# Performance work log

Measured on AMD Instinct MI355X. Metric: run time of the kernel, lower is better.

## Reference

```python
import jax, jax.numpy as jnp
import numpy as np

N_NODES = 50000
N_EDGES = 1600000
IN_DIM = 64 + 2 + 64   # protein + spatial + lri
HID = 64
OUT_DIM = 32
NUM_GRAPHS = 64
NEG_SLOPE = 0.2  # PyG GATConv default negative_slope


def _gat(x, src, dst, W, a_src, a_dst, bias):
    """PyG-style GATConv: x' = xW per head, per-edge attention with
    LeakyReLU + scatter-softmax over incoming edges, weighted scatter-sum.
    Heads are concatenated (concat=True default)."""
    N = x.shape[0]
    H, C = a_src.shape
    xp = (x @ W).reshape(N, H, C)                      # [N,H,C]
    al_src = jnp.sum(xp * a_src, axis=-1)              # [N,H]
    al_dst = jnp.sum(xp * a_dst, axis=-1)              # [N,H]
    e = jax.nn.leaky_relu(al_src[src] + al_dst[dst], NEG_SLOPE)  # [E,H]
    # numerically stable segment softmax over edges grouped by dst
    m = jax.ops.segment_max(e, dst, num_segments=N)
    ex = jnp.exp(e - m[dst])
    denom = jax.ops.segment_sum(ex, dst, num_segments=N)
    alpha = ex / denom[dst]                            # [E,H]
    out = jax.ops.segment_sum(alpha[:, :, None] * xp[src], dst, num_segments=N)
    return out.reshape(N, H * C) + bias


def setup_inputs() -> dict:
    key = jax.random.key(0)
    ks = jax.random.split(key, 16)
    def glorot(k, shape):
        fan_in = shape[0] if len(shape) == 2 else shape[-1]
        return jax.random.normal(k, shape, dtype=jnp.float32) / np.sqrt(fan_in)
    inp = {
        "protein_expr": jax.random.normal(ks[0], (N_NODES, 64), dtype=jnp.float32),
        "spatial_pos": jax.random.uniform(ks[1], (N_NODES, 2), dtype=jnp.float32),
        "lri_feats": jax.random.normal(ks[2], (N_NODES, 64), dtype=jnp.float32),
        "edge_index": jax.random.randint(ks[3], (2, N_EDGES), 0, N_NODES, dtype=jnp.int64),
        "batch": jnp.sort(jax.random.randint(ks[4], (N_NODES,), 0, NUM_GRAPHS, dtype=jnp.int64)),
        # encoder1: GATConv(IN_DIM -> HID, heads=2)
        "W1": glorot(ks[5], (IN_DIM, 2 * HID)),
        "a_src1": glorot(ks[6], (2, HID)),
        "a_dst1": glorot(ks[7], (2, HID)),
        "b1": jnp.zeros((2 * HID,), dtype=jnp.float32),
        # encoder2: GATConv(2*HID -> HID, heads=1)
        "W2": glorot(ks[8], (2 * HID, HID)),
        "a_src2": glorot(ks[9], (1, HID)),
        "a_dst2": glorot(ks[10], (1, HID)),
        "b2": jnp.zeros((HID,), dtype=jnp.float32),
        # decoder MLP
        "Wd1": glorot(ks[11], (HID, HID)),
        "bd1": jnp.zeros((HID,), dtype=jnp.float32),
        "Wd2": glorot(ks[12], (HID, OUT_DIM)),
        "bd2": jnp.zeros((OUT_DIM,), dtype=jnp.float32),
    }
    return inp


def reference(protein_expr, spatial_pos, lri_feats, edge_index, batch,
              W1, a_src1, a_dst1, b1, W2, a_src2, a_dst2, b2,
              Wd1, bd1, Wd2, bd2):
    N = protein_expr.shape[0]
    x = jnp.concatenate([protein_expr, spatial_pos, lri_feats], axis=1)  # [N, IN_DIM]
    # PyG GATConv adds self-loops by default
    loop = jnp.arange(N, dtype=edge_index.dtype)
    src = jnp.concatenate([edge_index[0], loop])
    dst = jnp.concatenate([edge_index[1], loop])
    h = _gat(x, src, dst, W1, a_src1, a_dst1, b1)   # [N, 2*HID]
    h = _gat(h, src, dst, W2, a_src2, a_dst2, b2)   # [N, HID]
    # global_mean_pool
    counts = jax.ops.segment_sum(jnp.ones((N,), h.dtype), batch, num_segments=NUM_GRAPHS)
    pooled = jax.ops.segment_sum(h, batch, num_segments=NUM_GRAPHS) / jnp.clip(counts, 1.0)[:, None]
    # decoder MLP
    d = jax.nn.relu(pooled @ Wd1 + bd1)
    return d @ Wd2 + bd2
```

## Files before the change

kernel.cpp:

```cpp
#include <hip/hip_runtime.h>
#include <hip/hip_bf16.h>

#define N_NODESC 50000
#define N_EDGESC 1600000
#define NUM_GRAPHSC 64
#define P_EPB 2048
#define SUBW 196
#define NSB 256
#define SBCAP 8192
#define POOL_REP 32
#define AGG_NB 6250

typedef __hip_bfloat16 bf16;
typedef short short8 __attribute__((ext_vector_type(8)));
typedef float floatx4 __attribute__((ext_vector_type(4)));

__device__ __forceinline__ float ldf(const void* p, long i, int fp32) {
    return fp32 ? ((const float*)p)[i] : __bfloat162float(((const bf16*)p)[i]);
}
__device__ __forceinline__ short f2s(float v) {
    bf16 h = __float2bfloat16(v);
    return *(short*)&h;
}
__device__ __forceinline__ unsigned pack2(float lo, float hi) {
    bf16 a = __float2bfloat16(lo), b = __float2bfloat16(hi);
    unsigned ua = *(unsigned short*)&a, ub = *(unsigned short*)&b;
    return (ub << 16) | ua;
}
__device__ __forceinline__ float ulo(unsigned u) { return __uint_as_float(u << 16); }
__device__ __forceinline__ float uhi(unsigned u) { return __uint_as_float(u & 0xffff0000u); }

__global__ void detect_k(const void* __restrict__ prot,
                         const void* __restrict__ eidx,
                         int* __restrict__ flags) {
    if (blockIdx.x == 0 && threadIdx.x == 0) {
        const bf16* pb = (const bf16*)prot;
        int sane = 0;
        for (int i = 0; i < 64; ++i) {
            float a = fabsf(__bfloat162float(pb[2 * i]));
            if (a > 1e-8f && a < 1e4f) sane++;
        }
        flags[0] = (sane >= 48) ? 0 : 1;
        const unsigned* u = (const unsigned*)eidx;
        int zhi = 0;
        for (int i = 0; i < 32; ++i)
            if (u[2 * i + 1] == 0u) zhi++;
        flags[1] = (zhi >= 30) ? 1 : 0;
    }
}

__global__ __launch_bounds__(256) void prep2_k(const void* __restrict__ W1,
                                               const void* __restrict__ W2,
                                               const int* __restrict__ flags,
                                               short* __restrict__ w1f,
                                               float* __restrict__ w1r,
                                               short* __restrict__ w2f,
                                               int* __restrict__ zreg, int nzero, int nzblk,
                                               const void* __restrict__ batch,
                                               int* __restrict__ b32) {
    const int fp32 = flags[0];
    const int b = blockIdx.x, tid = threadIdx.x;
    if (b < 64) {
        int idx = b * 256 + tid;
        int kp = idx >> 7, n = idx & 127;
        int krow = kp < 64 ? kp : 66 + (kp - 64);
        float v = ldf(W1, (long)krow * 128 + n, fp32);
        int c = n >> 4, nn = n & 15, t = kp >> 5, q = (kp >> 3) & 3, j = kp & 7;
        w1f[(((c * 4 + t) * 4 + q) * 16 + nn) * 8 + j] = f2s(v);
    } else if (b == 64) {
        int which = tid >> 7, n = tid & 127;
        w1r[which * 128 + n] = ldf(W1, (long)(64 + which) * 128 + n, fp32);
    } else if (b < 97) {
        int idx = (b - 65) * 256 + tid;
        int k = idx >> 6, n = idx & 63;
        float v = ldf(W2, (long)k * 64 + n, fp32);
        int c = n >> 4, nn = n & 15, t = k >> 5, q = (k >> 3) & 3, j = k & 7;
        w2f[(((c * 4 + t) * 4 + q) * 16 + nn) * 8 + j] = f2s(v);
    } else if (b < 97 + nzblk) {
        int i = (b - 97) * 256 + tid;
        if (i < nzero) zreg[i] = 0;
    } else {
        const int i64f = flags[1];
        int i = (b - 97 - nzblk) * 256 + tid;
        if (i < N_NODESC)
            b32[i] = i64f ? (int)((const long long*)batch)[i] : ((const int*)batch)[i];
    }
}

__global__ __launch_bounds__(256) void part_k(const void* __restrict__ eidx,
                                              const int* __restrict__ flags,
                                              int* __restrict__ scnt,
                                              unsigned* __restrict__ bucket2) {
    const int i64f = flags[1];
    const int tid = threadIdx.x;
    const long e0 = (long)blockIdx.x * P_EPB;
    __shared__ int cnt[NSB + 1];
    __shared__ int sc[NSB];
    __shared__ int gbase[NSB];
    __shared__ int cur[NSB];
    __shared__ unsigned buf[P_EPB];
    cnt[tid] = 0;
    if (tid == 0) cnt[NSB] = 0;
    __syncthreads();
    unsigned ev[8];
    int bk[8];
    #pragma unroll
    for (int i = 0; i < 8; ++i) {
        long e = e0 + i * 256 + tid;
        bk[i] = -1;
        if (e < N_EDGESC) {
            int s, d;
            if (i64f) {
                s = (int)((const long long*)eidx)[e];
                d = (int)((const long long*)eidx)[N_EDGESC + e];
            } else {
                s = ((const int*)eidx)[e];
                d = ((const int*)eidx)[N_EDGESC + e];
            }
            int sub = (d >> 2) / 49;
            bk[i] = sub;
            ev[i] = (unsigned)s | ((unsigned)(d - sub * SUBW) << 16);
            atomicAdd(&cnt[sub], 1);
        }
    }
    __syncthreads();
    const int myc = cnt[tid];
    sc[tid] = myc;
    __syncthreads();
    for (int off = 1; off < NSB; off <<= 1) {
        int t = (tid >= off) ? sc[tid - off] : 0;
        __syncthreads();
        sc[tid] += t;
        __syncthreads();
    }
    cnt[tid] = sc[tid] - myc;
    if (tid == NSB - 1) cnt[NSB] = sc[NSB - 1];
    gbase[tid] = myc ? atomicAdd(&scnt[tid], myc) : 0;
    cur[tid] = sc[tid] - myc;
    __syncthreads();
    #pragma unroll
    for (int i = 0; i < 8; ++i) {
        if (bk[i] >= 0) {
            int p = atomicAdd(&cur[bk[i]], 1);
            buf[p] = ev[i];
        }
    }
    __syncthreads();
    const int total = cnt[NSB];
    for (int p = tid; p < total; p += 256) {
        int lo = 0, hi = NSB;
        while (hi - lo > 1) { int mid = (lo + hi) >> 1; if (p >= cnt[mid]) lo = mid; else hi = mid; }
        bucket2[(long)lo * SBCAP + gbase[lo] + (p - cnt[lo])] = buf[p];
    }
}

__global__ __launch_bounds__(256) void csr_k(const unsigned* __restrict__ bucket2,
                                             const int* __restrict__ scnt,
                                             int* __restrict__ state,
                                             int* __restrict__ row_start,
                                             unsigned short* __restrict__ col) {
    const int sb = blockIdx.x;
    const int tid = threadIdx.x;
    const int lane = tid & 63;
    const int cnt = scnt[sb];
    const unsigned* B = bucket2 + (long)sb * SBCAP;
    __shared__ int lh[SUBW];
    __shared__ int sc[256];
    __shared__ int sprefix_sh;
    const int nodebase = sb * SUBW;
    const int width = min(SUBW, N_NODESC - nodebase);
    for (int i = tid; i < SUBW; i += 256) lh[i] = 0;
    __syncthreads();
    for (int e = tid; e < cnt; e += 256) atomicAdd(&lh[B[e] >> 16], 1);
    __syncthreads();
    const int myc = (tid < SUBW) ? lh[tid] : 0;
    sc[tid] = myc;
    __syncthreads();
    for (int off = 1; off < 256; off <<= 1) {
        int t = (tid >= off) ? sc[tid - off] : 0;
        __syncthreads();
        sc[tid] += t;
        __syncthreads();
    }
    const int total = sc[255];
    if (tid == 0)
        __hip_atomic_store(&state[sb], (int)((1u << 30) | (unsigned)total),
                           __ATOMIC_RELEASE, __HIP_MEMORY_SCOPE_AGENT);
    if (tid < 64) {
        int prefix = 0;
        if (sb > 0) {
            int base = sb;
            for (;;) {
                int t = base - 1 - lane;
                int v = 0;
                if (t >= 0) {
                    for (;;) {
                        v = __hip_atomic_load(&state[t], __ATOMIC_ACQUIRE,
                                              __HIP_MEMORY_SCOPE_AGENT);
                        if ((unsigned)v >= (1u << 30)) break;
                        __builtin_amdgcn_s_sleep(1);
                    }
                }
                int flag = (int)(((unsigned)v) >> 30);
                int val = v & 0x3fffffff;
                unsigned long long pmask = __ballot(flag == 2 && t >= 0);
                int stop_tid = pmask ? (__ffsll((long long)pmask) - 1) : 64;
                int contrib = 0;
                if (t >= 0 && lane <= stop_tid) contrib = val;
                #pragma unroll
                for (int off = 32; off; off >>= 1) contrib += __shfl_xor(contrib, off, 64);
                prefix += contrib;
                if (pmask || base <= 64) break;
                base -= 64;
            }
        }
        if (tid == 0) {
            sprefix_sh = prefix;
            __hip_atomic_store(&state[sb],
                               (int)((2u << 30) | (unsigned)(prefix + total)),
                               __ATOMIC_RELEASE, __HIP_MEMORY_SCOPE_AGENT);
        }
    }
    __syncthreads();
    const int sprefix = sprefix_sh;
    if (tid < width) row_start[nodebase + tid] = sprefix + sc[tid] - myc;
    if (sb == NSB - 1 && tid == 0) row_start[N_NODESC] = sprefix + total;
    if (tid < SUBW) lh[tid] = sprefix + sc[tid] - myc;
    __syncthreads();
    for (int e = tid; e < cnt; e += 256) {
        unsigned v = B[e];
        int pos = atomicAdd(&lh[v >> 16], 1);
        col[pos] = (unsigned short)(v & 0xffffu);
    }
}


__global__ __launch_bounds__(256) void gemm1_k(
        const void* __restrict__ prot, const void* __restrict__ sp,
        const void* __restrict__ lri,
        const short* __restrict__ w1f, const float* __restrict__ w1r,
        const void* __restrict__ as1, const void* __restrict__ ad1,
        const int* __restrict__ flags,
        short* __restrict__ xph0, short* __restrict__ xph1,
        float* __restrict__ alsrc, float* __restrict__ aldst) {
    const int fp32 = flags[0];
    const int tid = threadIdx.x;
    const int nb = blockIdx.x * 32;
    __shared__ __align__(16) short xs[32][136];
    __shared__ float xsp[32][2];
    __shared__ float sredc[32][8], dredc[32][8];

    if (!fp32) {
        #pragma unroll
        for (int i = 0; i < 2; ++i) {
            int cidx = i * 256 + tid;
            int r = cidx >> 4, cc = cidx & 15;
            int g = nb + r;
            short8 v = (short8){0, 0, 0, 0, 0, 0, 0, 0};
            if (g < N_NODESC) {
                const short* srcp = (cc < 8)
                    ? (const short*)prot + (long)g * 64 + cc * 8
                    : (const short*)lri + (long)g * 64 + (cc - 8) * 8;
                v = *(const short8*)srcp;
            }
            *(short8*)&xs[r][cc * 8] = v;
        }
    } else {
        #pragma unroll
        for (int i = 0; i < 16; ++i) {
            int idx = i * 256 + tid;
            int r = idx >> 7, k = idx & 127;
            int g = nb + r;
            float v = 0.f;
            if (g < N_NODESC)
                v = (k < 64) ? ((const float*)prot)[(long)g * 64 + k]
                             : ((const float*)lri)[(long)g * 64 + (k - 64)];
            xs[r][k] = f2s(v);
        }
    }
    if (tid < 64) {
        int r = tid >> 1, which = tid & 1;
        int g = nb + r;
        xsp[r][which] = (g < N_NODESC) ? ldf(sp, (long)g * 2 + which, fp32) : 0.f;
    }
    __syncthreads();

    const int wid = tid >> 6, lane = tid & 63;
    const int quad = lane >> 4, l16 = lane & 15;
    floatx4 acc[2][2];
    #pragma unroll
    for (int a = 0; a < 2; ++a)
        #pragma unroll
        for (int b = 0; b < 2; ++b) acc[a][b] = (floatx4){0.f, 0.f, 0.f, 0.f};

    const int c0 = 2 * wid;
    #pragma unroll
    for (int t = 0; t < 4; ++t) {
        short8 a0 = *(const short8*)&xs[l16][t * 32 + quad * 8];
        short8 a1 = *(const short8*)&xs[16 + l16][t * 32 + quad * 8];
        short8 b0 = *(const short8*)&w1f[(((c0 * 4 + t) * 4 + quad) * 16 + l16) * 8];
        short8 b1 = *(const short8*)&w1f[((((c0 + 1) * 4 + t) * 4 + quad) * 16 + l16) * 8];
        acc[0][0] = __builtin_amdgcn_mfma_f32_16x16x32_bf16(a0, b0, acc[0][0], 0, 0, 0);
        acc[0][1] = __builtin_amdgcn_mfma_f32_16x16x32_bf16(a0, b1, acc[0][1], 0, 0, 0);
        acc[1][0] = __builtin_amdgcn_mfma_f32_16x16x32_bf16(a1, b0, acc[1][0], 0, 0, 0);
        acc[1][1] = __builtin_amdgcn_mfma_f32_16x16x32_bf16(a1, b1, acc[1][1], 0, 0, 0);
    }
    #pragma unroll
    for (int ci = 0; ci < 2; ++ci) {
        int colg = (c0 + ci) * 16 + l16;
        float w0 = w1r[colg], w1v = w1r[128 + colg];
        float asv = ldf(as1, colg, fp32), adv = ldf(ad1, colg, fp32);
        short* xpd = (colg < 64) ? xph0 : xph1;
        const int cc = colg & 63;
        #pragma unroll
        for (int rt = 0; rt < 2; ++rt) {
            float sv[4], dv[4];
            #pragma unroll
            for (int reg = 0; reg < 4; ++reg) {
                int row = rt * 16 + quad * 4 + reg;
                int g = nb + row;
                float v = acc[rt][ci][reg] + xsp[row][0] * w0 + xsp[row][1] * w1v;
                if (g < N_NODESC) xpd[(long)g * 64 + cc] = f2s(v);
                sv[reg] = v * asv;
                dv[reg] = v * adv;
            }
            #pragma unroll
            for (int off = 1; off < 16; off <<= 1) {
                #pragma unroll
                for (int reg = 0; reg < 4; ++reg) {
                    sv[reg] += __shfl_xor(sv[reg], off, 64);
                    dv[reg] += __shfl_xor(dv[reg], off, 64);
                }
            }
            if (l16 == 0) {
                #pragma unroll
                for (int reg = 0; reg < 4; ++reg) {
                    int row = rt * 16 + quad * 4 + reg;
                    sredc[row][c0 + ci] = sv[reg];
                    dredc[row][c0 + ci] = dv[reg];
                }
            }
        }
    }
    __syncthreads();
    if (tid < 64) {
        int r = tid >> 1, h = tid & 1;
        int g = nb + r;
        if (g < N_NODESC) {
            alsrc[(long)h * N_NODESC + g] = sredc[r][4 * h] + sredc[r][4 * h + 1] +
                                            sredc[r][4 * h + 2] + sredc[r][4 * h + 3];
            aldst[(long)h * N_NODESC + g] = dredc[r][4 * h] + dredc[r][4 * h + 1] +
                                            dredc[r][4 * h + 2] + dredc[r][4 * h + 3];
        }
    }
}


__global__ __launch_bounds__(256) void agg1s_k(
        const int* __restrict__ row_start, const unsigned short* __restrict__ col,
        const short* __restrict__ xph0, const short* __restrict__ xph1,
        const float* __restrict__ als, const float* __restrict__ ald,
        const void* __restrict__ b1, const int* __restrict__ flags,
        unsigned* __restrict__ h1b32) {
    const int fp32 = flags[0];
    const int tid = threadIdx.x;
    const int wid = tid >> 6;
    const int lane = tid & 63;
    const int hw = lane >> 5;
    const int hl = lane & 31;
    const int head = blockIdx.x >= AGG_NB;
    const int b = blockIdx.x - head * AGG_NB;
    const int n = b * 8 + wid * 2 + hw;
    __shared__ float2 pbuf[4][2][32];
    float2* mybuf = pbuf[wid][hw];
    const short* xph = head ? xph1 : xph0;
    const float* alsh = als + (long)head * N_NODESC;
    const float* aldh = ald + (long)head * N_NODESC;
    const int e = hl >> 3;
    const int c = hl & 7;
    const char* xpb = (const char*)xph;
    const int c16 = c * 16;
    const float ad = aldh[n];
    float e0 = alsh[n] + ad;
    e0 = e0 > 0.f ? e0 : 0.2f * e0;
    const float pself = __expf(e0);
    const float pinit = e == 0 ? pself : 0.f;
    uint4 us = *(const uint4*)(xpb + (long)n * 128 + c16);
    float acc0 = pinit * ulo(us.x), acc1 = pinit * uhi(us.x);
    float acc2 = pinit * ulo(us.y), acc3 = pinit * uhi(us.y);
    float acc4 = pinit * ulo(us.z), acc5 = pinit * uhi(us.z);
    float acc6 = pinit * ulo(us.w), acc7 = pinit * uhi(us.w);
    float lp = 0.f;
    const int beg = row_start[n], end = row_start[n + 1];
    for (int base = beg; base < end; base += 32) {
        const int idx = base + hl;
        int s = 0;
        float p = 0.f;
        if (idx < end) {
            s = (int)col[idx];
            float t = alsh[s] + ad;
            t = t > 0.f ? t : 0.2f * t;
            p = __expf(t);
        }
        lp += p;
        mybuf[hl] = make_float2(p, __int_as_float(s << 7));
        int cnt = end - base; if (cnt > 32) cnt = 32;
        int quads = (cnt + 3) >> 2;
        int j = 0;
        for (; j + 4 <= quads; j += 4) {
            int a4[4]; float p4[4]; uint4 x[4];
            #pragma unroll
            for (int q = 0; q < 4; ++q) {
                float2 bv = mybuf[4 * (j + q) + e];
                a4[q] = __float_as_int(bv.y);
                p4[q] = bv.x;
            }
            #pragma unroll
            for (int q = 0; q < 4; ++q)
                x[q] = *(const uint4*)(xpb + a4[q] + c16);
            #pragma unroll
            for (int q = 0; q < 4; ++q) {
                acc0 = fmaf(p4[q], ulo(x[q].x), acc0);
                acc1 = fmaf(p4[q], uhi(x[q].x), acc1);
                acc2 = fmaf(p4[q], ulo(x[q].y), acc2);
                acc3 = fmaf(p4[q], uhi(x[q].y), acc3);
                acc4 = fmaf(p4[q], ulo(x[q].z), acc4);
                acc5 = fmaf(p4[q], uhi(x[q].z), acc5);
                acc6 = fmaf(p4[q], ulo(x[q].w), acc6);
                acc7 = fmaf(p4[q], uhi(x[q].w), acc7);
            }
        }
        for (; j < quads; ++j) {
            float2 bv = mybuf[4 * j + e];
            uint4 x = *(const uint4*)(xpb + __float_as_int(bv.y) + c16);
            float pv = bv.x;
            acc0 = fmaf(pv, ulo(x.x), acc0);
            acc1 = fmaf(pv, uhi(x.x), acc1);
            acc2 = fmaf(pv, ulo(x.y), acc2);
            acc3 = fmaf(pv, uhi(x.y), acc3);
            acc4 = fmaf(pv, ulo(x.z), acc4);
            acc5 = fmaf(pv, uhi(x.z), acc5);
            acc6 = fmaf(pv, ulo(x.w), acc6);
            acc7 = fmaf(pv, uhi(x.w), acc7);
        }
    }
    #pragma unroll
    for (int off = 16; off; off >>= 1) lp += __shfl_xor(lp, off, 64);
    #pragma unroll
    for (int off = 8; off <= 16; off <<= 1) {
        acc0 += __shfl_xor(acc0, off, 64);
        acc1 += __shfl_xor(acc1, off, 64);
        acc2 += __shfl_xor(acc2, off, 64);
        acc3 += __shfl_xor(acc3, off, 64);
        acc4 += __shfl_xor(acc4, off, 64);
        acc5 += __shfl_xor(acc5, off, 64);
        acc6 += __shfl_xor(acc6, off, 64);
        acc7 += __shfl_xor(acc7, off, 64);
    }
    if (hl < 8) {
        const float rl = 1.f / (lp + pself);
        const long bb = (long)head * 64 + 8 * c;
        float o0 = acc0 * rl + ldf(b1, bb + 0, fp32);
        float o1 = acc1 * rl + ldf(b1, bb + 1, fp32);
        float o2 = acc2 * rl + ldf(b1, bb + 2, fp32);
        float o3 = acc3 * rl + ldf(b1, bb + 3, fp32);
        float o4 = acc4 * rl + ldf(b1, bb + 4, fp32);
        float o5 = acc5 * rl + ldf(b1, bb + 5, fp32);
        float o6 = acc6 * rl + ldf(b1, bb + 6, fp32);
        float o7 = acc7 * rl + ldf(b1, bb + 7, fp32);
        uint4 o;
        o.x = pack2(o0, o1); o.y = pack2(o2, o3);
        o.z = pack2(o4, o5); o.w = pack2(o6, o7);
        *(uint4*)((char*)h1b32 + (long)n * 256 + head * 128 + c16) = o;
    }
}


__global__ __launch_bounds__(256) void gemm2_k(
        const unsigned* __restrict__ h1b32, const short* __restrict__ w2f,
        const void* __restrict__ as2, const void* __restrict__ ad2,
        const int* __restrict__ flags,
        short* __restrict__ xp2b, float* __restrict__ alsrc, float* __restrict__ aldst) {
    const int fp32 = flags[0];
    const int tid = threadIdx.x;
    const int nb = blockIdx.x * 32;
    __shared__ __align__(16) short xs[32][136];
    __shared__ float sredc[32][4], dredc[32][4];

    #pragma unroll
    for (int i = 0; i < 8; ++i) {
        int idx = i * 256 + tid;
        int r = idx >> 6, ii = idx & 63;
        int g = nb + r;
        unsigned val = (g < N_NODESC) ? h1b32[(long)g * 64 + ii] : 0u;
        ((unsigned*)&xs[r][0])[ii] = val;
    }
    __syncthreads();

    const int wid = tid >> 6, lane = tid & 63;
    const int quad = lane >> 4, l16 = lane & 15;
    floatx4 acc0 = (floatx4){0.f, 0.f, 0.f, 0.f};
    floatx4 acc1 = (floatx4){0.f, 0.f, 0.f, 0.f};
    #pragma unroll
    for (int t = 0; t < 4; ++t) {
        short8 a0 = *(const short8*)&xs[l16][t * 32 + quad * 8];
        short8 a1 = *(const short8*)&xs[16 + l16][t * 32 + quad * 8];
        short8 b = *(const short8*)&w2f[(((wid * 4 + t) * 4 + quad) * 16 + l16) * 8];
        acc0 = __builtin_amdgcn_mfma_f32_16x16x32_bf16(a0, b, acc0, 0, 0, 0);
        acc1 = __builtin_amdgcn_mfma_f32_16x16x32_bf16(a1, b, acc1, 0, 0, 0);
    }
    const int colg = wid * 16 + l16;
    const float asv = ldf(as2, colg, fp32), adv = ldf(ad2, colg, fp32);
    float sv0[4], dv0[4], sv1[4], dv1[4];
    #pragma unroll
    for (int reg = 0; reg < 4; ++reg) {
        int r0 = quad * 4 + reg;
        int g0 = nb + r0;
        int g1 = g0 + 16;
        if (g0 < N_NODESC) xp2b[(long)g0 * 64 + colg] = f2s(acc0[reg]);
        if (g1 < N_NODESC) xp2b[(long)g1 * 64 + colg] = f2s(acc1[reg]);
        sv0[reg] = acc0[reg] * asv; dv0[reg] = acc0[reg] * adv;
        sv1[reg] = acc1[reg] * asv; dv1[reg] = acc1[reg] * adv;
    }
    #pragma unroll
    for (int off = 1; off < 16; off <<= 1) {
        #pragma unroll
        for (int reg = 0; reg < 4; ++reg) {
            sv0[reg] += __shfl_xor(sv0[reg], off, 64);
            dv0[reg] += __shfl_xor(dv0[reg], off, 64);
            sv1[reg] += __shfl_xor(sv1[reg], off, 64);
            dv1[reg] += __shfl_xor(dv1[reg], off, 64);
        }
    }
    if (l16 == 0) {
        #pragma unroll
        for (int reg = 0; reg < 4; ++reg) {
            int r0 = quad * 4 + reg;
            sredc[r0][wid] = sv0[reg];      dredc[r0][wid] = dv0[reg];
            sredc[r0 + 16][wid] = sv1[reg]; dredc[r0 + 16][wid] = dv1[reg];
        }
    }
    __syncthreads();
    if (tid < 32) {
        int g = nb + tid;
        if (g < N_NODESC) {
            alsrc[g] = sredc[tid][0] + sredc[tid][1] + sredc[tid][2] + sredc[tid][3];
            aldst[g] = dredc[tid][0] + dredc[tid][1] + dredc[tid][2] + dredc[tid][3];
        }
    }
}


__global__ __launch_bounds__(256) void agg2p_k(
        const int* __restrict__ row_start, const unsigned short* __restrict__ col,
        const short* __restrict__ xp2b, const float* __restrict__ alsrc,
        const float* __restrict__ aldst, const void* __restrict__ b2v,
        const int* __restrict__ flags, const int* __restrict__ batch32,
        float* __restrict__ pooled, float* __restrict__ counts) {
    const int fp32 = flags[0];
    const int tid = threadIdx.x;
    const int wid = tid >> 6;
    const int lane = tid & 63;
    const int hw = lane >> 5;
    const int hl = lane & 31;
    const int n = blockIdx.x * 8 + wid * 2 + hw;
    const int rep = blockIdx.x & (POOL_REP - 1);
    __shared__ float2 pbuf[4][2][32];
    __shared__ float psum[64];
    __shared__ int ginfo[2];
    if (tid < 64) psum[tid] = 0.f;
    if (tid == 0) {
        int g0 = batch32[blockIdx.x * 8];
        int g7 = batch32[blockIdx.x * 8 + 7];
        ginfo[0] = g0;
        ginfo[1] = (g0 == g7);
    }
    __syncthreads();
    float2* mybuf = pbuf[wid][hw];
    const int e = hl >> 3;
    const int c = hl & 7;
    const char* xpb = (const char*)xp2b;
    const int c16 = c * 16;
    const float ad = aldst[n];
    float e0 = alsrc[n] + ad;
    e0 = e0 > 0.f ? e0 : 0.2f * e0;
    const float pself = __expf(e0);
    const float pinit = e == 0 ? pself : 0.f;
    uint4 us = *(const uint4*)(xpb + (long)n * 128 + c16);
    float acc0 = pinit * ulo(us.x), acc1 = pinit * uhi(us.x);
    float acc2 = pinit * ulo(us.y), acc3 = pinit * uhi(us.y);
    float acc4 = pinit * ulo(us.z), acc5 = pinit * uhi(us.z);
    float acc6 = pinit * ulo(us.w), acc7 = pinit * uhi(us.w);
    float lp = 0.f;
    const int beg = row_start[n], end = row_start[n + 1];
    for (int base = beg; base < end; base += 32) {
        const int idx = base + hl;
        int s = 0;
        float p = 0.f;
        if (idx < end) {
            s = (int)col[idx];
            float t = alsrc[s] + ad;
            t = t > 0.f ? t : 0.2f * t;
            p = __expf(t);
        }
        lp += p;
        mybuf[hl] = make_float2(p, __int_as_float(s << 7));
        int cnt = end - base; if (cnt > 32) cnt = 32;
        int quads = (cnt + 3) >> 2;
        int j = 0;
        for (; j + 4 <= quads; j += 4) {
            int a4[4]; float p4[4]; uint4 x[4];
            #pragma unroll
            for (int q = 0; q < 4; ++q) {
                float2 bv = mybuf[4 * (j + q) + e];
                a4[q] = __float_as_int(bv.y);
                p4[q] = bv.x;
            }
            #pragma unroll
            for (int q = 0; q < 4; ++q)
                x[q] = *(const uint4*)(xpb + a4[q] + c16);
            #pragma unroll
            for (int q = 0; q < 4; ++q) {
                acc0 = fmaf(p4[q], ulo(x[q].x), acc0);
                acc1 = fmaf(p4[q], uhi(x[q].x), acc1);
                acc2 = fmaf(p4[q], ulo(x[q].y), acc2);
                acc3 = fmaf(p4[q], uhi(x[q].y), acc3);
                acc4 = fmaf(p4[q], ulo(x[q].z), acc4);
                acc5 = fmaf(p4[q], uhi(x[q].z), acc5);
                acc6 = fmaf(p4[q], ulo(x[q].w), acc6);
                acc7 = fmaf(p4[q], uhi(x[q].w), acc7);
            }
        }
        for (; j < quads; ++j) {
            float2 bv = mybuf[4 * j + e];
            uint4 x = *(const uint4*)(xpb + __float_as_int(bv.y) + c16);
            float pv = bv.x;
            acc0 = fmaf(pv, ulo(x.x), acc0);
            acc1 = fmaf(pv, uhi(x.x), acc1);
            acc2 = fmaf(pv, ulo(x.y), acc2);
            acc3 = fmaf(pv, uhi(x.y), acc3);
            acc4 = fmaf(pv, ulo(x.z), acc4);
            acc5 = fmaf(pv, uhi(x.z), acc5);
            acc6 = fmaf(pv, ulo(x.w), acc6);
            acc7 = fmaf(pv, uhi(x.w), acc7);
        }
    }
    #pragma unroll
    for (int off = 16; off; off >>= 1) lp += __shfl_xor(lp, off, 64);
    #pragma unroll
    for (int off = 8; off <= 16; off <<= 1) {
        acc0 += __shfl_xor(acc0, off, 64);
        acc1 += __shfl_xor(acc1, off, 64);
        acc2 += __shfl_xor(acc2, off, 64);
        acc3 += __shfl_xor(acc3, off, 64);
        acc4 += __shfl_xor(acc4, off, 64);
        acc5 += __shfl_xor(acc5, off, 64);
        acc6 += __shfl_xor(acc6, off, 64);
        acc7 += __shfl_xor(acc7, off, 64);
    }
    float o[8];
    if (hl < 8) {
        const float rl = 1.f / (lp + pself);
        o[0] = acc0 * rl + ldf(b2v, 8 * c + 0, fp32);
        o[1] = acc1 * rl + ldf(b2v, 8 * c + 1, fp32);
        o[2] = acc2 * rl + ldf(b2v, 8 * c + 2, fp32);
        o[3] = acc3 * rl + ldf(b2v, 8 * c + 3, fp32);
        o[4] = acc4 * rl + ldf(b2v, 8 * c + 4, fp32);
        o[5] = acc5 * rl + ldf(b2v, 8 * c + 5, fp32);
        o[6] = acc6 * rl + ldf(b2v, 8 * c + 6, fp32);
        o[7] = acc7 * rl + ldf(b2v, 8 * c + 7, fp32);
    }
    if (ginfo[1]) {
        if (hl < 8) {
            #pragma unroll
            for (int j = 0; j < 8; ++j) atomicAdd(&psum[8 * c + j], o[j]);
        }
        __syncthreads();
        if (tid < 64)
            atomicAdd(&pooled[((long)rep * NUM_GRAPHSC + ginfo[0]) * 64 + tid], psum[tid]);
        if (tid == 0) atomicAdd(&counts[rep * NUM_GRAPHSC + ginfo[0]], 8.f);
    } else {
        int g = batch32[n];
        if (hl < 8) {
            #pragma unroll
            for (int j = 0; j < 8; ++j)
                atomicAdd(&pooled[((long)rep * NUM_GRAPHSC + g) * 64 + 8 * c + j], o[j]);
        }
        if (hl == 0) atomicAdd(&counts[rep * NUM_GRAPHSC + g], 1.f);
    }
}


__global__ __launch_bounds__(64) void dec_k(const float* __restrict__ pooled,
                                            const float* __restrict__ counts,
                                            const void* __restrict__ Wd1, const void* __restrict__ bd1,
                                            const void* __restrict__ Wd2, const void* __restrict__ bd2,
                                            const int* __restrict__ flags,
                                            void* __restrict__ out) {
    const int fp32 = flags[0];
    const int g = blockIdx.x, j = threadIdx.x;
    __shared__ float p[64], dh[64];
    float cnt = 0.f, ps = 0.f;
    #pragma unroll
    for (int r = 0; r < POOL_REP; ++r) {
        ps += pooled[((long)r * NUM_GRAPHSC + g) * 64 + j];
        if (j == 0) cnt += counts[r * NUM_GRAPHSC + g];
    }
    __shared__ float cnt_sh;
    if (j == 0) cnt_sh = cnt < 1.f ? 1.f : cnt;
    __syncthreads();
    p[j] = ps / cnt_sh;
    __syncthreads();
    float acc = ldf(bd1, j, fp32);
    for (int k = 0; k < 64; ++k) acc += p[k] * ldf(Wd1, k * 64 + j, fp32);
    dh[j] = acc > 0.f ? acc : 0.f;
    __syncthreads();
    if (j < 32) {
        float o = ldf(bd2, j, fp32);
        for (int k = 0; k < 64; ++k) o += dh[k] * ldf(Wd2, k * 32 + j, fp32);
        if (fp32) ((float*)out)[g * 32 + j] = o;
        else      ((bf16*)out)[g * 32 + j] = __float2bfloat16(o);
    }
}

extern "C" void kernel_launch(void* const* d_in, const int* in_sizes, int n_in,
                              void* d_out, int out_size, void* d_ws, size_t ws_size,
                              hipStream_t stream) {
    (void)in_sizes; (void)n_in; (void)out_size; (void)ws_size;
    const void* prot = d_in[0];
    const void* sp   = d_in[1];
    const void* lri  = d_in[2];
    const void* eidx = d_in[3];
    const void* batch= d_in[4];
    const void* W1   = d_in[5];
    const void* as1  = d_in[6];
    const void* ad1  = d_in[7];
    const void* b1   = d_in[8];
    const void* W2   = d_in[9];
    const void* as2  = d_in[10];
    const void* ad2  = d_in[11];
    const void* b2v  = d_in[12];
    const void* Wd1  = d_in[13];
    const void* bd1  = d_in[14];
    const void* Wd2  = d_in[15];
    const void* bd2  = d_in[16];

    char* w = (char*)d_ws;
    auto alloc = [&](size_t bytes) -> void* {
        char* p = w;
        w += (bytes + 255) & ~(size_t)255;
        return (void*)p;
    };
    int*   flags     = (int*)alloc(2 * 4);
    float* pooled    = (float*)alloc((size_t)POOL_REP * NUM_GRAPHSC * 64 * 4);
    float* counts    = (float*)alloc((size_t)POOL_REP * NUM_GRAPHSC * 4);
    int*   scnt      = (int*)alloc((size_t)NSB * 4);
    int*   state     = (int*)alloc((size_t)NSB * 4);
    char*  zero_end  = w;
    int*   batch32   = (int*)alloc((size_t)N_NODESC * 4);
    int*   row_start = (int*)alloc((size_t)(N_NODESC + 1) * 4);
    unsigned* bucket2= (unsigned*)alloc((size_t)NSB * SBCAP * 4);
    unsigned short* col = (unsigned short*)alloc((size_t)N_EDGESC * 2);
    short* w1f       = (short*)alloc((size_t)16384 * 2);
    float* w1r       = (float*)alloc((size_t)256 * 4);
    short* w2f       = (short*)alloc((size_t)8192 * 2);
    short* xph0      = (short*)alloc((size_t)N_NODESC * 64 * 2);
    short* xph1      = (short*)alloc((size_t)N_NODESC * 64 * 2);
    float* alsrc1    = (float*)alloc((size_t)N_NODESC * 2 * 4);
    float* aldst1    = (float*)alloc((size_t)N_NODESC * 2 * 4);
    short* h1b       = (short*)alloc((size_t)N_NODESC * 128 * 2);
    short* xp2b      = (short*)alloc((size_t)N_NODESC * 64 * 2);
    float* alsrc2    = (float*)alloc((size_t)N_NODESC * 4);
    float* aldst2    = (float*)alloc((size_t)N_NODESC * 4);

    const int nzero = (int)((zero_end - (char*)pooled) / 4);
    const int nzblk = (nzero + 255) / 256;
    const int nbat  = (N_NODESC + 255) / 256;

    detect_k<<<1, 64, 0, stream>>>(prot, eidx, flags);
    prep2_k<<<97 + nzblk + nbat, 256, 0, stream>>>(W1, W2, flags, w1f, w1r, w2f,
                                                   (int*)pooled, nzero, nzblk,
                                                   batch, batch32);
    part_k<<<(N_EDGESC + P_EPB - 1) / P_EPB, 256, 0, stream>>>(eidx, flags, scnt, bucket2);
    csr_k<<<NSB, 256, 0, stream>>>(bucket2, scnt, state, row_start, col);

    const int nblk = (N_NODESC + 31) / 32;
    gemm1_k<<<nblk, 256, 0, stream>>>(prot, sp, lri, w1f, w1r, as1, ad1, flags,
                                      xph0, xph1, alsrc1, aldst1);
    agg1s_k<<<2 * AGG_NB, 256, 0, stream>>>(row_start, col, xph0, xph1,
                                            alsrc1, aldst1, b1, flags,
                                            (unsigned*)h1b);
    gemm2_k<<<nblk, 256, 0, stream>>>((const unsigned*)h1b, w2f, as2, ad2, flags,
                                      xp2b, alsrc2, aldst2);
    agg2p_k<<<AGG_NB, 256, 0, stream>>>(row_start, col, xp2b, alsrc2, aldst2,
                                        b2v, flags, batch32, pooled, counts);
    dec_k<<<NUM_GRAPHSC, 64, 0, stream>>>(pooled, counts, Wd1, bd1, Wd2, bd2, flags, d_out);
}
```

Before: 314.3 us.

## Merge setup kernels and fuse CSR build with first GEMM launch

Folds detection, weight prep, batch conversion and edge partitioning into one kernel, and runs the CSR build blocks alongside the first GEMM blocks in a single launch. Zeroing moves to a hipMemsetAsync call. Each partitioned edge now carries its bucket id in its top bits, which removes the per-element binary search in the scatter. This cuts launch count and inter-kernel gaps, at the cost of blocks re-running the format detection redundantly and CSR blocks sharing a grid with GEMM blocks that may delay the decoupled-lookback chain.

```diff
diff --git a/kernel.cpp b/kernel.cpp
--- a/kernel.cpp
+++ b/kernel.cpp
@@ -5,6 +5,7 @@
 #define N_EDGESC 1600000
 #define NUM_GRAPHSC 64
 #define P_EPB 2048
+#define NPART ((N_EDGESC + P_EPB - 1) / P_EPB)
 #define SUBW 196
 #define NSB 256
 #define SBCAP 8192
@@ -30,212 +31,146 @@
 __device__ __forceinline__ float ulo(unsigned u) { return __uint_as_float(u << 16); }
 __device__ __forceinline__ float uhi(unsigned u) { return __uint_as_float(u & 0xffff0000u); }
 
-__global__ void detect_k(const void* __restrict__ prot,
-                         const void* __restrict__ eidx,
-                         int* __restrict__ flags) {
-    if (blockIdx.x == 0 && threadIdx.x == 0) {
-        const bf16* pb = (const bf16*)prot;
-        int sane = 0;
-        for (int i = 0; i < 64; ++i) {
-            float a = fabsf(__bfloat162float(pb[2 * i]));
-            if (a > 1e-8f && a < 1e4f) sane++;
-        }
-        flags[0] = (sane >= 48) ? 0 : 1;
-        const unsigned* u = (const unsigned*)eidx;
-        int zhi = 0;
-        for (int i = 0; i < 32; ++i)
-            if (u[2 * i + 1] == 0u) zhi++;
-        flags[1] = (zhi >= 30) ? 1 : 0;
-    }
-}
-
-__global__ __launch_bounds__(256) void prep2_k(const void* __restrict__ W1,
-                                               const void* __restrict__ W2,
-                                               const int* __restrict__ flags,
-                                               short* __restrict__ w1f,
-                                               float* __restrict__ w1r,
-                                               short* __restrict__ w2f,
-                                               int* __restrict__ zreg, int nzero, int nzblk,
-                                               const void* __restrict__ batch,
-                                               int* __restrict__ b32) {
-    const int fp32 = flags[0];
+__device__ __forceinline__ int detect_fp32_dev(const void* prot) {
+    const bf16* pb = (const bf16*)prot;
+    int sane = 0;
+    for (int i = 0; i < 64; ++i) {
+        float a = fabsf(__bfloat162float(pb[2 * i]));
+        if (a > 1e-8f && a < 1e4f) sane++;
+    }
+    return (sane >= 48) ? 0 : 1;
+}
+__device__ __forceinline__ int detect_i64_dev(const void* eidx) {
+    const unsigned* u = (const unsigned*)eidx;
+    int zhi = 0;
+    for (int i = 0; i < 32; ++i)
+        if (u[2 * i + 1] == 0u) zhi++;
+    return (zhi >= 30) ? 1 : 0;
+}
+
+__global__ __launch_bounds__(256) void mega_k(const void* __restrict__ eidx,
+                                              const void* __restrict__ prot,
+                                              const void* __restrict__ batch,
+                                              const void* __restrict__ W1,
+                                              const void* __restrict__ W2,
+                                              int* __restrict__ flags,
+                                              short* __restrict__ w1f,
+                                              float* __restrict__ w1r,
+                                              short* __restrict__ w2f,
+                                              int* __restrict__ b32,
+                                              int* __restrict__ scnt,
+                                              unsigned* __restrict__ bucket2,
+                                              int nbat) {
     const int b = blockIdx.x, tid = threadIdx.x;
-    if (b < 64) {
-        int idx = b * 256 + tid;
-        int kp = idx >> 7, n = idx & 127;
-        int krow = kp < 64 ? kp : 66 + (kp - 64);
-        float v = ldf(W1, (long)krow * 128 + n, fp32);
-        int c = n >> 4, nn = n & 15, t = kp >> 5, q = (kp >> 3) & 3, j = kp & 7;
-        w1f[(((c * 4 + t) * 4 + q) * 16 + nn) * 8 + j] = f2s(v);
-    } else if (b == 64) {
-        int which = tid >> 7, n = tid & 127;
-        w1r[which * 128 + n] = ldf(W1, (long)(64 + which) * 128 + n, fp32);
-    } else if (b < 97) {
-        int idx = (b - 65) * 256 + tid;
-        int k = idx >> 6, n = idx & 63;
-        float v = ldf(W2, (long)k * 64 + n, fp32);
-        int c = n >> 4, nn = n & 15, t = k >> 5, q = (k >> 3) & 3, j = k & 7;
-        w2f[(((c * 4 + t) * 4 + q) * 16 + nn) * 8 + j] = f2s(v);
-    } else if (b < 97 + nzblk) {
-        int i = (b - 97) * 256 + tid;
-        if (i < nzero) zreg[i] = 0;
-    } else {
-        const int i64f = flags[1];
-        int i = (b - 97 - nzblk) * 256 + tid;
-        if (i < N_NODESC)
-            b32[i] = i64f ? (int)((const long long*)batch)[i] : ((const int*)batch)[i];
-    }
-}
-
-__global__ __launch_bounds__(256) void part_k(const void* __restrict__ eidx,
-                                              const int* __restrict__ flags,
-                                              int* __restrict__ scnt,
-                                              unsigned* __restrict__ bucket2) {
-    const int i64f = flags[1];
-    const int tid = threadIdx.x;
-    const long e0 = (long)blockIdx.x * P_EPB;
-    __shared__ int cnt[NSB + 1];
+    __shared__ int cnt[NSB];
     __shared__ int sc[NSB];
     __shared__ int gbase[NSB];
     __shared__ int cur[NSB];
     __shared__ unsigned buf[P_EPB];
-    cnt[tid] = 0;
-    if (tid == 0) cnt[NSB] = 0;
+    __shared__ int sflag;
+
+    if (b < NPART) {
+        if (tid == 0) sflag = detect_i64_dev(eidx);
+        cnt[tid] = 0;
+        __syncthreads();
+        const int i64f = sflag;
+        const long e0 = (long)b * P_EPB;
+        unsigned ev[8];
+        int bk[8];
+        #pragma unroll
+        for (int i = 0; i < 8; ++i) {
+            long e = e0 + i * 256 + tid;
+            bk[i] = -1;
+            if (e < N_EDGESC) {
+                int s, d;
+                if (i64f) {
+                    s = (int)((const long long*)eidx)[e];
+                    d = (int)((const long long*)eidx)[N_EDGESC + e];
+                } else {
+                    s = ((const int*)eidx)[e];
+                    d = ((const int*)eidx)[N_EDGESC + e];
+                }
+                int sub = (d >> 2) / 49;
+                bk[i] = sub;
+                ev[i] = (unsigned)s | ((unsigned)(d - sub * SUBW) << 16)
+                                    | ((unsigned)sub << 24);
+                atomicAdd(&cnt[sub], 1);
+            }
+        }
+        __syncthreads();
+        const int myc = cnt[tid];
+        sc[tid] = myc;
+        __syncthreads();
+        #pragma unroll
+        for (int off = 1; off < NSB; off <<= 1) {
+            int t = (tid >= off) ? sc[tid - off] : 0;
+            __syncthreads();
+            sc[tid] += t;
+            __syncthreads();
+        }
+        cnt[tid] = sc[tid] - myc;
+        gbase[tid] = myc ? atomicAdd(&scnt[tid], myc) : 0;
+        cur[tid] = sc[tid] - myc;
+        __syncthreads();
+        #pragma unroll
+        for (int i = 0; i < 8; ++i) {
+            if (bk[i] >= 0) {
+                int p = atomicAdd(&cur[bk[i]], 1);
+                buf[p] = ev[i];
+            }
+        }
+        __syncthreads();
+        const int total = sc[NSB - 1];
+        for (int p = tid; p < total; p += 256) {
+            unsigned v = buf[p];
+            int lo = (int)(v >> 24);
+            bucket2[(long)lo * SBCAP + gbase[lo] + (p - cnt[lo])] = v & 0xffffffu;
+        }
+        return;
+    }
+    const int wb = b - NPART;
+    if (wb < 97) {
+        if (tid == 0) {
+            sflag = detect_fp32_dev(prot);
+            if (wb == 0) {
+                flags[0] = sflag;
+                flags[1] = detect_i64_dev(eidx);
+            }
+        }
+        __syncthreads();
+        const int fp32 = sflag;
+        if (wb < 64) {
+            int idx = wb * 256 + tid;
+            int kp = idx >> 7, n = idx & 127;
+            int krow = kp < 64 ? kp : 66 + (kp - 64);
+            float v = ldf(W1, (long)krow * 128 + n, fp32);
+            int c = n >> 4, nn = n & 15, t = kp >> 5, q = (kp >> 3) & 3, j = kp & 7;
+            w1f[(((c * 4 + t) * 4 + q) * 16 + nn) * 8 + j] = f2s(v);
+        } else if (wb == 64) {
+            int which = tid >> 7, n = tid & 127;
+            w1r[which * 128 + n] = ldf(W1, (long)(64 + which) * 128 + n, fp32);
+        } else {
+            int idx = (wb - 65) * 256 + tid;
+            int k = idx >> 6, n = idx & 63;
+            float v = ldf(W2, (long)k * 64 + n, fp32);
+            int c = n >> 4, nn = n & 15, t = k >> 5, q = (k >> 3) & 3, j = k & 7;
+            w2f[(((c * 4 + t) * 4 + q) * 16 + nn) * 8 + j] = f2s(v);
+        }
+        return;
+    }
+    if (tid == 0) sflag = detect_i64_dev(eidx);
     __syncthreads();
-    unsigned ev[8];
-    int bk[8];
-    #pragma unroll
-    for (int i = 0; i < 8; ++i) {
-        long e = e0 + i * 256 + tid;
-        bk[i] = -1;
-        if (e < N_EDGESC) {
-            int s, d;
-            if (i64f) {
-                s = (int)((const long long*)eidx)[e];
-                d = (int)((const long long*)eidx)[N_EDGESC + e];
-            } else {
-                s = ((const int*)eidx)[e];
-                d = ((const int*)eidx)[N_EDGESC + e];
-            }
-            int sub = (d >> 2) / 49;
-            bk[i] = sub;
-            ev[i] = (unsigned)s | ((unsigned)(d - sub * SUBW) << 16);
-            atomicAdd(&cnt[sub], 1);
-        }
-    }
-    __syncthreads();
-    const int myc = cnt[tid];
-    sc[tid] = myc;
-    __syncthreads();
-    for (int off = 1; off < NSB; off <<= 1) {
-        int t = (tid >= off) ? sc[tid - off] : 0;
-        __syncthreads();
-        sc[tid] += t;
-        __syncthreads();
-    }
-    cnt[tid] = sc[tid] - myc;
-    if (tid == NSB - 1) cnt[NSB] = sc[NSB - 1];
-    gbase[tid] = myc ? atomicAdd(&scnt[tid], myc) : 0;
-    cur[tid] = sc[tid] - myc;
-    __syncthreads();
-    #pragma unroll
-    for (int i = 0; i < 8; ++i) {
-        if (bk[i] >= 0) {
-            int p = atomicAdd(&cur[bk[i]], 1);
-            buf[p] = ev[i];
-        }
-    }
-    __syncthreads();
-    const int total = cnt[NSB];
-    for (int p = tid; p < total; p += 256) {
-        int lo = 0, hi = NSB;
-        while (hi - lo > 1) { int mid = (lo + hi) >> 1; if (p >= cnt[mid]) lo = mid; else hi = mid; }
-        bucket2[(long)lo * SBCAP + gbase[lo] + (p - cnt[lo])] = buf[p];
-    }
-}
-
-__global__ __launch_bounds__(256) void csr_k(const unsigned* __restrict__ bucket2,
-                                             const int* __restrict__ scnt,
-                                             int* __restrict__ state,
-                                             int* __restrict__ row_start,
-                                             unsigned short* __restrict__ col) {
-    const int sb = blockIdx.x;
-    const int tid = threadIdx.x;
-    const int lane = tid & 63;
-    const int cnt = scnt[sb];
-    const unsigned* B = bucket2 + (long)sb * SBCAP;
-    __shared__ int lh[SUBW];
-    __shared__ int sc[256];
-    __shared__ int sprefix_sh;
-    const int nodebase = sb * SUBW;
-    const int width = min(SUBW, N_NODESC - nodebase);
-    for (int i = tid; i < SUBW; i += 256) lh[i] = 0;
-    __syncthreads();
-    for (int e = tid; e < cnt; e += 256) atomicAdd(&lh[B[e] >> 16], 1);
-    __syncthreads();
-    const int myc = (tid < SUBW) ? lh[tid] : 0;
-    sc[tid] = myc;
-    __syncthreads();
-    for (int off = 1; off < 256; off <<= 1) {
-        int t = (tid >= off) ? sc[tid - off] : 0;
-        __syncthreads();
-        sc[tid] += t;
-        __syncthreads();
-    }
-    const int total = sc[255];
-    if (tid == 0)
-        __hip_atomic_store(&state[sb], (int)((1u << 30) | (unsigned)total),
-                           __ATOMIC_RELEASE, __HIP_MEMORY_SCOPE_AGENT);
-    if (tid < 64) {
-        int prefix = 0;
-        if (sb > 0) {
-            int base = sb;
-            for (;;) {
-                int t = base - 1 - lane;
-                int v = 0;
-                if (t >= 0) {
-                    for (;;) {
-                        v = __hip_atomic_load(&state[t], __ATOMIC_ACQUIRE,
-                                              __HIP_MEMORY_SCOPE_AGENT);
-                        if ((unsigned)v >= (1u << 30)) break;
-                        __builtin_amdgcn_s_sleep(1);
-                    }
-                }
-                int flag = (int)(((unsigned)v) >> 30);
-                int val = v & 0x3fffffff;
-                unsigned long long pmask = __ballot(flag == 2 && t >= 0);
-                int stop_tid = pmask ? (__ffsll((long long)pmask) - 1) : 64;
-                int contrib = 0;
-                if (t >= 0 && lane <= stop_tid) contrib = val;
-                #pragma unroll
-                for (int off = 32; off; off >>= 1) contrib += __shfl_xor(contrib, off, 64);
-                prefix += contrib;
-                if (pmask || base <= 64) break;
-                base -= 64;
-            }
-        }
-        if (tid == 0) {
-            sprefix_sh = prefix;
-            __hip_atomic_store(&state[sb],
-                               (int)((2u << 30) | (unsigned)(prefix + total)),
-                               __ATOMIC_RELEASE, __HIP_MEMORY_SCOPE_AGENT);
-        }
-    }
-    __syncthreads();
-    const int sprefix = sprefix_sh;
-    if (tid < width) row_start[nodebase + tid] = sprefix + sc[tid] - myc;
-    if (sb == NSB - 1 && tid == 0) row_start[N_NODESC] = sprefix + total;
-    if (tid < SUBW) lh[tid] = sprefix + sc[tid] - myc;
-    __syncthreads();
-    for (int e = tid; e < cnt; e += 256) {
-        unsigned v = B[e];
-        int pos = atomicAdd(&lh[v >> 16], 1);
-        col[pos] = (unsigned short)(v & 0xffffu);
-    }
-}
-
-
-__global__ __launch_bounds__(256) void gemm1_k(
+    const int i64f = sflag;
+    int i = (wb - 97) * 256 + tid;
+    if (i < N_NODESC)
+        b32[i] = i64f ? (int)((const long long*)batch)[i] : ((const int*)batch)[i];
+    (void)nbat;
+}
+
+__global__ __launch_bounds__(256) void csrgemm1_k(
+        const unsigned* __restrict__ bucket2, const int* __restrict__ scnt,
+        int* __restrict__ state, int* __restrict__ row_start,
+        unsigned short* __restrict__ col,
         const void* __restrict__ prot, const void* __restrict__ sp,
         const void* __restrict__ lri,
         const short* __restrict__ w1f, const float* __restrict__ w1r,
@@ -243,13 +178,89 @@
         const int* __restrict__ flags,
         short* __restrict__ xph0, short* __restrict__ xph1,
         float* __restrict__ alsrc, float* __restrict__ aldst) {
-    const int fp32 = flags[0];
     const int tid = threadIdx.x;
-    const int nb = blockIdx.x * 32;
+    __shared__ int lh[SUBW];
+    __shared__ int sc[256];
+    __shared__ int sprefix_sh;
     __shared__ __align__(16) short xs[32][136];
     __shared__ float xsp[32][2];
     __shared__ float sredc[32][8], dredc[32][8];
 
+    if (blockIdx.x < NSB) {
+        const int sb = blockIdx.x;
+        const int lane = tid & 63;
+        const int cnt = scnt[sb];
+        const unsigned* B = bucket2 + (long)sb * SBCAP;
+        const int nodebase = sb * SUBW;
+        const int width = min(SUBW, N_NODESC - nodebase);
+        for (int i = tid; i < SUBW; i += 256) lh[i] = 0;
+        __syncthreads();
+        for (int e = tid; e < cnt; e += 256) atomicAdd(&lh[B[e] >> 16], 1);
+        __syncthreads();
+        const int myc = (tid < SUBW) ? lh[tid] : 0;
+        sc[tid] = myc;
+        __syncthreads();
+        for (int off = 1; off < 256; off <<= 1) {
+            int t = (tid >= off) ? sc[tid - off] : 0;
+            __syncthreads();
+            sc[tid] += t;
+            __syncthreads();
+        }
+        const int total = sc[255];
+        if (tid == 0)
+            __hip_atomic_store(&state[sb], (int)((1u << 30) | (unsigned)total),
+                               __ATOMIC_RELEASE, __HIP_MEMORY_SCOPE_AGENT);
+        if (tid < 64) {
+            int prefix = 0;
+            if (sb > 0) {
+                int base = sb;
+                for (;;) {
+                    int t = base - 1 - lane;
+                    int v = 0;
+                    if (t >= 0) {
+                        for (;;) {
+                            v = __hip_atomic_load(&state[t], __ATOMIC_ACQUIRE,
+                                                  __HIP_MEMORY_SCOPE_AGENT);
+                            if ((unsigned)v >= (1u << 30)) break;
+                            __builtin_amdgcn_s_sleep(1);
+                        }
+                    }
+                    int flag = (int)(((unsigned)v) >> 30);
+                    int val = v & 0x3fffffff;
+                    unsigned long long pmask = __ballot(flag == 2 && t >= 0);
+                    int stop_tid = pmask ? (__ffsll((long long)pmask) - 1) : 64;
+                    int contrib = 0;
+                    if (t >= 0 && lane <= stop_tid) contrib = val;
+                    #pragma unroll
+                    for (int off = 32; off; off >>= 1) contrib += __shfl_xor(contrib, off, 64);
+                    prefix += contrib;
+                    if (pmask || base <= 64) break;
+                    base -= 64;
+                }
+            }
+            if (tid == 0) {
+                sprefix_sh = prefix;
+                __hip_atomic_store(&state[sb],
+                                   (int)((2u << 30) | (unsigned)(prefix + total)),
+                                   __ATOMIC_RELEASE, __HIP_MEMORY_SCOPE_AGENT);
+            }
+        }
+        __syncthreads();
+        const int sprefix = sprefix_sh;
+        if (tid < width) row_start[nodebase + tid] = sprefix + sc[tid] - myc;
+        if (sb == NSB - 1 && tid == 0) row_start[N_NODESC] = sprefix + total;
+        if (tid < SUBW) lh[tid] = sprefix + sc[tid] - myc;
+        __syncthreads();
+        for (int e = tid; e < cnt; e += 256) {
+            unsigned v = B[e];
+            int pos = atomicAdd(&lh[v >> 16], 1);
+            col[pos] = (unsigned short)(v & 0xffffu);
+        }
+        return;
+    }
+
+    const int fp32 = flags[0];
+    const int nb = (blockIdx.x - NSB) * 32;
     if (!fp32) {
         #pragma unroll
         for (int i = 0; i < 2; ++i) {
@@ -291,7 +302,7 @@
     #pragma unroll
     for (int a = 0; a < 2; ++a)
         #pragma unroll
-        for (int b = 0; b < 2; ++b) acc[a][b] = (floatx4){0.f, 0.f, 0.f, 0.f};
+        for (int bb = 0; bb < 2; ++bb) acc[a][bb] = (floatx4){0.f, 0.f, 0.f, 0.f};
 
     const int c0 = 2 * wid;
     #pragma unroll
@@ -773,20 +784,17 @@
     float* alsrc2    = (float*)alloc((size_t)N_NODESC * 4);
     float* aldst2    = (float*)alloc((size_t)N_NODESC * 4);
 
-    const int nzero = (int)((zero_end - (char*)pooled) / 4);
-    const int nzblk = (nzero + 255) / 256;
-    const int nbat  = (N_NODESC + 255) / 256;
-
-    detect_k<<<1, 64, 0, stream>>>(prot, eidx, flags);
-    prep2_k<<<97 + nzblk + nbat, 256, 0, stream>>>(W1, W2, flags, w1f, w1r, w2f,
-                                                   (int*)pooled, nzero, nzblk,
-                                                   batch, batch32);
-    part_k<<<(N_EDGESC + P_EPB - 1) / P_EPB, 256, 0, stream>>>(eidx, flags, scnt, bucket2);
-    csr_k<<<NSB, 256, 0, stream>>>(bucket2, scnt, state, row_start, col);
-
+    const int nbat = (N_NODESC + 255) / 256;
+    const size_t zero_bytes = (size_t)(zero_end - (char*)pooled);
+
+    hipMemsetAsync(pooled, 0, zero_bytes, stream);
+    mega_k<<<NPART + 97 + nbat, 256, 0, stream>>>(eidx, prot, batch, W1, W2, flags,
+                                                  w1f, w1r, w2f, batch32, scnt,
+                                                  bucket2, nbat);
     const int nblk = (N_NODESC + 31) / 32;
-    gemm1_k<<<nblk, 256, 0, stream>>>(prot, sp, lri, w1f, w1r, as1, ad1, flags,
-                                      xph0, xph1, alsrc1, aldst1);
+    csrgemm1_k<<<NSB + nblk, 256, 0, stream>>>(bucket2, scnt, state, row_start, col,
+                                               prot, sp, lri, w1f, w1r, as1, ad1,
+                                               flags, xph0, xph1, alsrc1, aldst1);
     agg1s_k<<<2 * AGG_NB, 256, 0, stream>>>(row_start, col, xph0, xph1,
                                             alsrc1, aldst1, b1, flags,
                                             (unsigned*)h1b);
```

After: 302.6 us. 3.7% less time.
